# Optimization experiments

Hardware: AMD Instinct MI355X
Metric: run time of the kernel (lower is better)

Reference implementation:

```python
import jax, jax.numpy as jnp
import numpy as np

IMAGE_W = 1024
IMAGE_H = 1024
STRIDES = (8, 16, 32, 64, 128)
TOP_N = 1000
MIN_SCORE = 0.05
NMS_THR = 0.6
MAX_DET = 100
NEG = -1e9  # sentinel for suppressed scores


def _positions(stride):
    # Faithful to repo: shifts_x indexed by feature_h, shifts_y by feature_w,
    # grid built [hf, wf, 2] = [shift_x_i, shift_y_j], then permute(1,0,2).
    hf, wf = IMAGE_H // stride, IMAGE_W // stride
    sx = (jnp.arange(hf, dtype=jnp.float32) + 0.5) * stride
    sy = (jnp.arange(wf, dtype=jnp.float32) + 0.5) * stride
    pos = jnp.stack(jnp.meshgrid(sx, sy, indexing='ij'), axis=-1)  # [hf, wf, 2]
    return jnp.transpose(pos, (1, 0, 2)).reshape(-1, 2)  # [hf*wf, 2]


def _filter_level(cls_h, reg_h, ctr_h, pos):
    B, C = cls_h.shape[0], cls_h.shape[-1]
    cls_h = jax.nn.sigmoid(cls_h).reshape(B, -1, C)
    reg_h = jnp.exp(reg_h).reshape(B, -1, 4)
    ctr_h = jax.nn.sigmoid(ctr_h).reshape(B, -1)
    scores = jnp.max(cls_h, axis=-1)
    classes = jnp.argmax(cls_h, axis=-1).astype(jnp.int32)
    scores = jnp.sqrt(scores * ctr_h)
    N = scores.shape[1]
    if N >= TOP_N:
        scores, idx = jax.lax.top_k(scores, TOP_N)  # sorted descending, like torch.topk
        classes = jnp.take_along_axis(classes, idx, axis=1)
        reg_h = jnp.take_along_axis(reg_h, idx[..., None], axis=1)
        posb = pos[idx]  # [B, TOP_N, 2]
    else:
        posb = jnp.broadcast_to(pos[None], (B, N, 2))
    return scores, classes, reg_h, posb


def _snap(reg, pos):
    # reg: [B, N, 4] (l,t,r,b), pos: [B, N, 2]
    b = jnp.concatenate([pos - reg[:, :, 0:2], pos + reg[:, :, 2:4]], axis=-1)
    b = b.astype(jnp.int32)  # torch .int() truncation
    b = jnp.stack([
        jnp.maximum(b[..., 0], 0),
        jnp.maximum(b[..., 1], 0),
        jnp.minimum(b[..., 2], IMAGE_W - 1),
        jnp.minimum(b[..., 3], IMAGE_H - 1),
    ], axis=-1)
    return b.astype(jnp.float32)


def _nms_image(scores, classes, boxes):
    # scores [N], classes [N] int32, boxes [N,4] float (already snapped to int grid)
    s = jnp.where(scores > MIN_SCORE, scores, NEG)
    x1, y1, x2, y2 = boxes[:, 0], boxes[:, 1], boxes[:, 2], boxes[:, 3]
    areas = (x2 - x1) * (y2 - y1)
    out_s = -jnp.ones((MAX_DET,), jnp.float32)
    out_c = -jnp.ones((MAX_DET,), jnp.float32)
    out_b = -jnp.ones((MAX_DET, 4), jnp.float32)

    def body(i, st):
        s, os_, oc, ob = st
        idx = jnp.argmax(s)            # highest remaining score -> sorted keep order
        ok = s[idx] > MIN_SCORE        # any un-suppressed valid candidate left?
        bb = boxes[idx]
        iw = jnp.clip(jnp.minimum(x2, bb[2]) - jnp.maximum(x1, bb[0]), 0.0)
        ih = jnp.clip(jnp.minimum(y2, bb[3]) - jnp.maximum(y1, bb[1]), 0.0)
        inter = iw * ih
        iou = inter / (areas + areas[idx] - inter + 1e-12)
        s = jnp.where((iou > NMS_THR) & ok, NEG, s)
        s = s.at[idx].set(NEG)
        os_ = os_.at[i].set(jnp.where(ok, scores[idx], -1.0))
        oc = oc.at[i].set(jnp.where(ok, classes[idx].astype(jnp.float32), -1.0))
        ob = ob.at[i].set(jnp.where(ok, bb, -jnp.ones((4,), jnp.float32)))
        return (s, os_, oc, ob)

    _, os_, oc, ob = jax.lax.fori_loop(0, MAX_DET, body, (s, out_s, out_c, out_b))
    return os_, oc, ob


def _decode(cls_heads, reg_heads, ctr_heads):
    sc_l, cl_l, rg_l, ps_l = [], [], [], []
    for c, r, t, st in zip(cls_heads, reg_heads, ctr_heads, STRIDES):
        sc, cl, rg, ps = _filter_level(c, r, t, _positions(st))
        sc_l.append(sc); cl_l.append(cl); rg_l.append(rg); ps_l.append(ps)
    scores = jnp.concatenate(sc_l, axis=1)
    classes = jnp.concatenate(cl_l, axis=1)
    regs = jnp.concatenate(rg_l, axis=1)
    poss = jnp.concatenate(ps_l, axis=1)
    boxes = _snap(regs, poss)
    return jax.vmap(_nms_image)(scores, classes, boxes)


def setup_inputs() -> dict:
    key = jax.random.key(0)
    ks = jax.random.split(key, 15)
    B, C = 8, 80
    sizes = [IMAGE_H // s for s in STRIDES]
    inp = {}
    for i, hw in enumerate(sizes):
        inp[f'cls{i}'] = jax.random.normal(ks[i], (B, hw, hw, C), dtype=jnp.float32)
        # +3 so exp(reg) gives realistic ~20px extents
        inp[f'reg{i}'] = jax.random.normal(ks[5 + i], (B, hw, hw, 4), dtype=jnp.float32) + 3.0
        inp[f'ctr{i}'] = jax.random.normal(ks[10 + i], (B, hw, hw, 1), dtype=jnp.float32)
    return inp


def reference(cls0, cls1, cls2, cls3, cls4,
              reg0, reg1, reg2, reg3, reg4,
              ctr0, ctr1, ctr2, ctr3, ctr4):
    cls_heads = [cls0, cls1, cls2, cls3, cls4]
    reg_heads = [reg0, reg1, reg2, reg3, reg4]
    ctr_heads = [ctr0, ctr1, ctr2, ctr3, ctr4]
    batch_scores, batch_classes, batch_boxes = _decode(cls_heads, reg_heads, ctr_heads)
    return batch_scores, batch_classes, batch_boxes
```

## Files before the change

kernel.cpp:

```cpp
#include <hip/hip_runtime.h>

#define NPOS 21824
#define MINS 0.05f
#define BT   1024
#define NW   (BT/64)

struct Ptrs { const float* cls[5]; const float* reg[5]; const float* ctr[5]; };

__device__ __forceinline__ float sigf(float x){ return 1.0f/(1.0f+expf(-x)); }

__device__ __forceinline__ unsigned long long mkkey(unsigned int b, int p){
    return ((unsigned long long)b << 16) | (unsigned)(65535 - p);
}

__global__ __launch_bounds__(256) void k_score(Ptrs P, float* scoreAll, int* clsAll,
                                               float4* boxAll)
{
    int img  = blockIdx.y;
    int blk  = blockIdx.x;
    int tid  = threadIdx.x;
    int posb = tid >> 2;
    int l    = tid & 3;
    int p    = blk*64 + posb;
    int lvl, base, lw, stride;
    if (blk < 256)      { lvl=0; base=0;     lw=7; stride=8;   }
    else if (blk < 320) { lvl=1; base=16384; lw=6; stride=16;  }
    else if (blk < 336) { lvl=2; base=20480; lw=5; stride=32;  }
    else if (blk < 340) { lvl=3; base=21504; lw=4; stride=64;  }
    else                { lvl=4; base=21760; lw=3; stride=128; }
    int pl = p - base;
    int h = pl >> lw, w = pl & ((1<<lw)-1);
    long long lidx = (long long)img*(1<<(2*lw)) + pl;

    const float4* c4 = (const float4*)(P.cls[lvl] + lidx*80);
    float mx = -3.4e38f; int mi = 0;
#pragma unroll
    for (int j = 0; j < 5; ++j) {
        int k = j*4 + l;
        float4 v = c4[k];
        int cb = k*4;
        if (v.x > mx){mx=v.x; mi=cb;}
        if (v.y > mx){mx=v.y; mi=cb+1;}
        if (v.z > mx){mx=v.z; mi=cb+2;}
        if (v.w > mx){mx=v.w; mi=cb+3;}
    }
#pragma unroll
    for (int d = 1; d < 4; d <<= 1) {
        float omx = __shfl_xor(mx, d);
        int   omi = __shfl_xor(mi, d);
        if (omx > mx || (omx == mx && omi < mi)) { mx = omx; mi = omi; }
    }
    if (l == 0) {
        float ct = P.ctr[lvl][lidx];
        float sc = sqrtf(sigf(mx)*sigf(ct));
        float4 rg = ((const float4*)P.reg[lvl])[lidx];
        float x = (w + 0.5f)*(float)stride;
        float y = (h + 0.5f)*(float)stride;
        int ix1 = (int)(x - expf(rg.x));
        int iy1 = (int)(y - expf(rg.y));
        int ix2 = (int)(x + expf(rg.z));
        int iy2 = (int)(y + expf(rg.w));
        ix1 = max(ix1,0); iy1 = max(iy1,0);
        ix2 = min(ix2,1023); iy2 = min(iy2,1023);
        int o = img*NPOS + p;
        scoreAll[o] = sc;
        clsAll[o]   = mi;
        boxAll[o]   = make_float4((float)ix1,(float)iy1,(float)ix2,(float)iy2);
    }
}

__device__ void radix24(const unsigned int* vals, int N, int K,
                        int* histA, int* histB, int* wsum,
                        unsigned int* shPref, int* shK, int tid)
{
    for (int i = tid; i < N; i += BT)
        atomicAdd(&histA[vals[i] >> 19], 1);
    __syncthreads();
    {
        int lo = tid*2;
        int ls = histA[lo] + histA[lo+1];
        int lane = tid & 63, wv = tid >> 6;
        int v = ls;
#pragma unroll
        for (int off = 1; off < 64; off <<= 1) {
            int o = __shfl_down(v, off);
            if (lane + off < 64) v += o;
        }
        if (lane == 0) wsum[wv] = v;
        __syncthreads();
        int add = 0;
        for (int q = wv + 1; q < NW; ++q) add += wsum[q];
        int mine = v + add;
        int above = mine - ls;
        if (above < K && mine >= K) {
            if (above + histA[lo+1] >= K) { *shPref = (unsigned)(lo+1) << 19; *shK = K - above; }
            else { *shPref = (unsigned)lo << 19; *shK = K - above - histA[lo+1]; }
        }
        __syncthreads();
    }
    unsigned int pref = *shPref;
    int K2 = *shK;
    for (int i = tid; i < N; i += BT) {
        unsigned int b = vals[i];
        if ((b >> 19) == (pref >> 19)) atomicAdd(&histB[(b >> 8) & 2047], 1);
    }
    __syncthreads();
    {
        int lo = tid*2;
        int ls = histB[lo] + histB[lo+1];
        int lane = tid & 63, wv = tid >> 6;
        int v = ls;
#pragma unroll
        for (int off = 1; off < 64; off <<= 1) {
            int o = __shfl_down(v, off);
            if (lane + off < 64) v += o;
        }
        if (lane == 0) wsum[wv] = v;
        __syncthreads();
        int add = 0;
        for (int q = wv + 1; q < NW; ++q) add += wsum[q];
        int mine = v + add;
        int above = mine - ls;
        if (above < K2 && mine >= K2) {
            if (above + histB[lo+1] >= K2) { *shPref = pref | ((unsigned)(lo+1) << 8); *shK = K2 - above; }
            else { *shPref = pref | ((unsigned)lo << 8); *shK = K2 - above - histB[lo+1]; }
        }
        __syncthreads();
    }
}

__global__ __launch_bounds__(BT) void k_nms(const float* scoreAll,
                                            const float4* boxAll, const int* clsAll,
                                            float* out)
{
    __shared__ int histA[2048], histB[2048], wsum[NW];
    __shared__ unsigned int shPref;
    __shared__ int shK, tick, eqn;
    __shared__ unsigned long long eqKey[1024];
    __shared__ unsigned long long sel[256];
    __shared__ unsigned long long sorted[256];
    __shared__ float4 sBox[256];
    __shared__ float  sCls[256];
    __shared__ __align__(16) unsigned long long sRow[256][4];
    __shared__ int accIdx[100];
    __shared__ float4 accBox[100];
    __shared__ int shNaM, shNa;
    __shared__ unsigned long long shLast;

    int img = blockIdx.x, tid = threadIdx.x;
    const unsigned int* gs = (const unsigned int*)scoreAll + (long long)img*NPOS;
    const float4* gBox = boxAll + (long long)img*NPOS;
    const int*    gCls = clsAll + (long long)img*NPOS;

    float* outS = out + img*100;
    float* outC = out + 800 + img*100;
    float* outB = out + 1600 + img*400;

    for (int i = tid; i < 2048; i += BT) { histA[i] = 0; histB[i] = 0; }
    if (tid == 0) { tick = 0; eqn = 0; }
    __syncthreads();

    radix24(gs, NPOS, 256, histA, histB, wsum, &shPref, &shK, tid);
    unsigned int kth = shPref >> 8;
    int need = shK;
    for (int i = tid; i < NPOS; i += BT) {
        unsigned int b = gs[i], hb = b >> 8;
        if (hb > kth)       { int t = atomicAdd(&tick, 1); sel[t] = mkkey(b, i); }
        else if (hb == kth) { int t = atomicAdd(&eqn, 1); if (t < 1024) eqKey[t] = mkkey(b, i); }
    }
    __syncthreads();
    int m = eqn, nG = tick;
    if (m <= 1024) {
        for (int q = tid; q < m; q += BT) {
            unsigned long long kq = eqKey[q];
            int r = 0;
            for (int j = 0; j < m; ++j) r += (eqKey[j] > kq);
            if (r < need) sel[nG + r] = kq;
        }
    } else if (tid == 0) {
        unsigned long long last = ~0ULL;
        for (int c = 0; c < need; ++c) {
            unsigned long long best = 0;
            for (int i = 0; i < NPOS; ++i) {
                unsigned int b = gs[i];
                if ((b >> 8) == kth) {
                    unsigned long long k2 = mkkey(b, i);
                    if (k2 < last && k2 > best) best = k2;
                }
            }
            sel[nG + c] = best; last = best;
        }
    }
    __syncthreads();

    if (tid < 256) {
        unsigned long long k = sel[tid];
        int r = 0;
        for (int j = 0; j < 256; ++j) r += (sel[j] > k);
        sorted[r] = k;
    }
    __syncthreads();
    if (tid < 256) {
        int p = 65535 - (int)(sorted[tid] & 0xFFFF);
        sBox[tid] = gBox[p];
        sCls[tid] = (float)gCls[p];
    }

    float myScore = 0.f;
    if (tid < 256) myScore = __uint_as_float((unsigned int)(sorted[tid] >> 16));
    int nValid = __syncthreads_count(myScore > MINS ? 1 : 0);

    {
        int row = tid & 255, qq = tid >> 8;
        float4 bi = sBox[row];
        float  ai = (bi.z-bi.x)*(bi.w-bi.y);
        unsigned long long mv = 0;
#pragma unroll 8
        for (int jj = 0; jj < 64; ++jj) {
            int j = qq*64 + jj;
            float4 bj = sBox[j];
            float aj = (bj.z-bj.x)*(bj.w-bj.y);
            float iw = fmaxf(fminf(bj.z,bi.z)-fmaxf(bj.x,bi.x),0.f);
            float ih = fmaxf(fminf(bj.w,bi.w)-fmaxf(bj.y,bi.y),0.f);
            float in_ = iw*ih;
            bool s = (j > row) && (in_/(aj+ai-in_+1e-12f) > 0.6f);
            mv |= ((unsigned long long)s) << jj;
        }
        sRow[row][qq] = mv;
    }
    __syncthreads();

    if (tid == 0) {
        int na = 0;
        unsigned long long r0=0, r1=0, r2=0, r3=0;
#define FCOS_WBLK(RW, IB)                                                  \
        {                                                                  \
            int hi = nValid < ((IB)+1)*64 ? nValid : ((IB)+1)*64;          \
            for (int i = (IB)*64; i < hi && na < 100; ++i) {               \
                if ((RW >> (i - (IB)*64)) & 1ull) continue;                \
                accIdx[na++] = i;                                          \
                const ulonglong2* rp = (const ulonglong2*)sRow[i];         \
                ulonglong2 ra = rp[0], rb = rp[1];                         \
                r0 |= ra.x; r1 |= ra.y; r2 |= rb.x; r3 |= rb.y;            \
            }                                                              \
        }
        FCOS_WBLK(r0,0) FCOS_WBLK(r1,1) FCOS_WBLK(r2,2) FCOS_WBLK(r3,3)
#undef FCOS_WBLK
        shNaM = na; shNa = na;
    }
    __syncthreads();

    int naM = shNaM;
    if (naM < 100 && nValid == 256) {
        if (tid < naM) accBox[tid] = sBox[accIdx[tid]];
        if (tid == 0) shLast = sorted[255];
        __syncthreads();
        while (true) {
            if (shNa >= 100) break;
            unsigned long long last = shLast;
            unsigned long long bk = 0;
            for (int i = tid; i < NPOS; i += BT) {
                unsigned long long k2 = mkkey(gs[i], i);
                if (k2 < last && k2 > bk) bk = k2;
            }
#pragma unroll
            for (int off = 32; off > 0; off >>= 1) {
                unsigned long long o = __shfl_down(bk, off);
                if (o > bk) bk = o;
            }
            int lane = tid & 63, wv = tid >> 6;
            if (lane == 0) eqKey[wv] = bk;
            __syncthreads();
            if (tid == 0) {
                unsigned long long best = 0;
                for (int q = 0; q < NW; ++q) if (eqKey[q] > best) best = eqKey[q];
                shLast = best;
            }
            __syncthreads();
            unsigned long long ck = shLast;
            if (ck == 0ULL) break;
            float sc = __uint_as_float((unsigned int)(ck >> 16));
            if (!(sc > MINS)) break;
            int p = 65535 - (int)(ck & 0xFFFF);
            float4 bb = gBox[p];
            float ba = (bb.z-bb.x)*(bb.w-bb.y);
            int na = shNa;
            bool mySup = false;
            if (tid < na) {
                float4 ab = accBox[tid];
                float aa = (ab.z-ab.x)*(ab.w-ab.y);
                float iw = fmaxf(fminf(bb.z,ab.z)-fmaxf(bb.x,ab.x),0.f);
                float ih = fmaxf(fminf(bb.w,ab.w)-fmaxf(bb.y,ab.y),0.f);
                float in_ = iw*ih;
                mySup = in_/(ba+aa-in_+1e-12f) > 0.6f;
            }
            int supCnt = __syncthreads_count(mySup);
            if (supCnt == 0) {
                if (tid == 0) {
                    int na2 = shNa;
                    outS[na2] = sc;
                    outC[na2] = (float)gCls[p];
                    outB[4*na2+0]=bb.x; outB[4*na2+1]=bb.y;
                    outB[4*na2+2]=bb.z; outB[4*na2+3]=bb.w;
                    accBox[na2] = bb;
                    shNa = na2 + 1;
                }
            }
            __syncthreads();
        }
    }
    __syncthreads();

    {
        int naM2 = shNaM, naT = shNa;
        if (tid < 100) {
            if (tid < naM2) {
                int r = accIdx[tid];
                unsigned long long k = sorted[r];
                float4 b = sBox[r];
                outS[tid] = __uint_as_float((unsigned int)(k >> 16));
                outC[tid] = sCls[r];
                outB[4*tid+0]=b.x; outB[4*tid+1]=b.y;
                outB[4*tid+2]=b.z; outB[4*tid+3]=b.w;
            } else if (tid >= naT) {
                outS[tid] = -1.f; outC[tid] = -1.f;
                outB[4*tid+0]=-1.f; outB[4*tid+1]=-1.f;
                outB[4*tid+2]=-1.f; outB[4*tid+3]=-1.f;
            }
        }
    }
}

extern "C" void kernel_launch(void* const* d_in, const int* in_sizes, int n_in,
                              void* d_out, int out_size, void* d_ws, size_t ws_size,
                              hipStream_t stream) {
    Ptrs P;
    bool interleaved = (in_sizes[1] == 8 * 128 * 128 * 4);
    for (int i = 0; i < 5; ++i) {
        if (interleaved) {
            P.cls[i] = (const float*)d_in[3*i];
            P.reg[i] = (const float*)d_in[3*i + 1];
            P.ctr[i] = (const float*)d_in[3*i + 2];
        } else {
            P.cls[i] = (const float*)d_in[i];
            P.reg[i] = (const float*)d_in[5 + i];
            P.ctr[i] = (const float*)d_in[10 + i];
        }
    }

    char* wbase = (char*)d_ws;
    size_t off = 0;
    auto alloc = [&](size_t bytes) -> void* {
        void* r = wbase + off;
        off += (bytes + 255) & ~(size_t)255;
        return r;
    };
    float*  scoreAll = (float*)alloc((size_t)8 * NPOS * 4);
    int*    clsAll   = (int*)alloc((size_t)8 * NPOS * 4);
    float4* boxAll   = (float4*)alloc((size_t)8 * NPOS * 16);

    dim3 gA(341, 8);
    k_score <<<gA, 256, 0, stream>>>(P, scoreAll, clsAll, boxAll);
    k_nms   <<<8, BT, 0, stream>>>(scoreAll, boxAll, clsAll, (float*)d_out);
}
```

Measured before the change: 159.7 us.

## Prefilter high-score candidates into a compact list and compute boxes lazily

The scoring kernel now appends keys for positions whose score exceeds a fixed 0.85 threshold to a per-image candidate list via a global atomic. The NMS kernel then runs its radix top-K selection over that short list instead of scanning all 21824 scores, and falls back to the full scan when the list holds fewer than 256 entries or overflows. Boxes are no longer precomputed and stored for every position; they are decoded from the regression input only for the selected candidates. This cuts global writes and the single-block scan cost, at the price of atomics in the score kernel, an extra memset, and a threshold tuned to the score distribution (the fallback keeps results correct).

Measured after the change: 241.2 us. 1.51x slower.

```diff
diff --git a/kernel.cpp b/kernel.cpp
--- a/kernel.cpp
+++ b/kernel.cpp
@@ -4,6 +4,8 @@
 #define MINS 0.05f
 #define BT   1024
 #define NW   (BT/64)
+#define TFAST 0.85f
+#define CAP  16384
 
 struct Ptrs { const float* cls[5]; const float* reg[5]; const float* ctr[5]; };
 
@@ -13,8 +15,30 @@
     return ((unsigned long long)b << 16) | (unsigned)(65535 - p);
 }
 
+__device__ __forceinline__ float4 computeBox(const Ptrs& P, int img, int p){
+    int base, lw, stride, lvl;
+    if (p < 16384)      { lvl=0; base=0;     lw=7; stride=8;   }
+    else if (p < 20480) { lvl=1; base=16384; lw=6; stride=16;  }
+    else if (p < 21504) { lvl=2; base=20480; lw=5; stride=32;  }
+    else if (p < 21760) { lvl=3; base=21504; lw=4; stride=64;  }
+    else                { lvl=4; base=21760; lw=3; stride=128; }
+    int pl = p - base;
+    int h = pl >> lw, w = pl & ((1<<lw)-1);
+    long long lidx = (long long)img*(1<<(2*lw)) + pl;
+    float4 rg = ((const float4*)P.reg[lvl])[lidx];
+    float x = (w + 0.5f)*(float)stride;
+    float y = (h + 0.5f)*(float)stride;
+    int ix1 = (int)(x - expf(rg.x));
+    int iy1 = (int)(y - expf(rg.y));
+    int ix2 = (int)(x + expf(rg.z));
+    int iy2 = (int)(y + expf(rg.w));
+    ix1 = max(ix1,0); iy1 = max(iy1,0);
+    ix2 = min(ix2,1023); iy2 = min(iy2,1023);
+    return make_float4((float)ix1,(float)iy1,(float)ix2,(float)iy2);
+}
+
 __global__ __launch_bounds__(256) void k_score(Ptrs P, float* scoreAll, int* clsAll,
-                                               float4* boxAll)
+                                               unsigned long long* list, int* listCnt)
 {
     int img  = blockIdx.y;
     int blk  = blockIdx.x;
@@ -22,14 +46,13 @@
     int posb = tid >> 2;
     int l    = tid & 3;
     int p    = blk*64 + posb;
-    int lvl, base, lw, stride;
-    if (blk < 256)      { lvl=0; base=0;     lw=7; stride=8;   }
-    else if (blk < 320) { lvl=1; base=16384; lw=6; stride=16;  }
-    else if (blk < 336) { lvl=2; base=20480; lw=5; stride=32;  }
-    else if (blk < 340) { lvl=3; base=21504; lw=4; stride=64;  }
-    else                { lvl=4; base=21760; lw=3; stride=128; }
+    int lvl, base, lw;
+    if (blk < 256)      { lvl=0; base=0;     lw=7; }
+    else if (blk < 320) { lvl=1; base=16384; lw=6; }
+    else if (blk < 336) { lvl=2; base=20480; lw=5; }
+    else if (blk < 340) { lvl=3; base=21504; lw=4; }
+    else                { lvl=4; base=21760; lw=3; }
     int pl = p - base;
-    int h = pl >> lw, w = pl & ((1<<lw)-1);
     long long lidx = (long long)img*(1<<(2*lw)) + pl;
 
     const float4* c4 = (const float4*)(P.cls[lvl] + lidx*80);
@@ -53,85 +76,47 @@
     if (l == 0) {
         float ct = P.ctr[lvl][lidx];
         float sc = sqrtf(sigf(mx)*sigf(ct));
-        float4 rg = ((const float4*)P.reg[lvl])[lidx];
-        float x = (w + 0.5f)*(float)stride;
-        float y = (h + 0.5f)*(float)stride;
-        int ix1 = (int)(x - expf(rg.x));
-        int iy1 = (int)(y - expf(rg.y));
-        int ix2 = (int)(x + expf(rg.z));
-        int iy2 = (int)(y + expf(rg.w));
-        ix1 = max(ix1,0); iy1 = max(iy1,0);
-        ix2 = min(ix2,1023); iy2 = min(iy2,1023);
         int o = img*NPOS + p;
         scoreAll[o] = sc;
         clsAll[o]   = mi;
-        boxAll[o]   = make_float4((float)ix1,(float)iy1,(float)ix2,(float)iy2);
-    }
-}
-
-__device__ void radix24(const unsigned int* vals, int N, int K,
-                        int* histA, int* histB, int* wsum,
-                        unsigned int* shPref, int* shK, int tid)
+        if (sc > TFAST) {
+            int t = atomicAdd(&listCnt[img], 1);
+            if (t < CAP) list[(long long)img*CAP + t] = mkkey(__float_as_uint(sc), p);
+        }
+    }
+}
+
+__device__ void suffix_pick(const int* hist, int* wsum, int K,
+                            unsigned int prefBase, int shift,
+                            unsigned int* shPref, int* shK, int tid)
 {
-    for (int i = tid; i < N; i += BT)
-        atomicAdd(&histA[vals[i] >> 19], 1);
-    __syncthreads();
-    {
-        int lo = tid*2;
-        int ls = histA[lo] + histA[lo+1];
-        int lane = tid & 63, wv = tid >> 6;
-        int v = ls;
+    int lo = tid*2;
+    int h0 = hist[lo], h1 = hist[lo+1];
+    int ls = h0 + h1;
+    int lane = tid & 63, wv = tid >> 6;
+    int v = ls;
 #pragma unroll
-        for (int off = 1; off < 64; off <<= 1) {
-            int o = __shfl_down(v, off);
-            if (lane + off < 64) v += o;
-        }
-        if (lane == 0) wsum[wv] = v;
-        __syncthreads();
-        int add = 0;
-        for (int q = wv + 1; q < NW; ++q) add += wsum[q];
-        int mine = v + add;
-        int above = mine - ls;
-        if (above < K && mine >= K) {
-            if (above + histA[lo+1] >= K) { *shPref = (unsigned)(lo+1) << 19; *shK = K - above; }
-            else { *shPref = (unsigned)lo << 19; *shK = K - above - histA[lo+1]; }
-        }
-        __syncthreads();
-    }
-    unsigned int pref = *shPref;
-    int K2 = *shK;
-    for (int i = tid; i < N; i += BT) {
-        unsigned int b = vals[i];
-        if ((b >> 19) == (pref >> 19)) atomicAdd(&histB[(b >> 8) & 2047], 1);
-    }
-    __syncthreads();
-    {
-        int lo = tid*2;
-        int ls = histB[lo] + histB[lo+1];
-        int lane = tid & 63, wv = tid >> 6;
-        int v = ls;
-#pragma unroll
-        for (int off = 1; off < 64; off <<= 1) {
-            int o = __shfl_down(v, off);
-            if (lane + off < 64) v += o;
-        }
-        if (lane == 0) wsum[wv] = v;
-        __syncthreads();
-        int add = 0;
-        for (int q = wv + 1; q < NW; ++q) add += wsum[q];
-        int mine = v + add;
-        int above = mine - ls;
-        if (above < K2 && mine >= K2) {
-            if (above + histB[lo+1] >= K2) { *shPref = pref | ((unsigned)(lo+1) << 8); *shK = K2 - above; }
-            else { *shPref = pref | ((unsigned)lo << 8); *shK = K2 - above - histB[lo+1]; }
-        }
-        __syncthreads();
-    }
-}
-
-__global__ __launch_bounds__(BT) void k_nms(const float* scoreAll,
-                                            const float4* boxAll, const int* clsAll,
-                                            float* out)
+    for (int off = 1; off < 64; off <<= 1) {
+        int o = __shfl_down(v, off);
+        if (lane + off < 64) v += o;
+    }
+    if (lane == 0) wsum[wv] = v;
+    __syncthreads();
+    int add = 0;
+    for (int q = wv + 1; q < NW; ++q) add += wsum[q];
+    int mine = v + add;
+    int above = mine - ls;
+    if (above < K && mine >= K) {
+        if (above + h1 >= K) { *shPref = prefBase | ((unsigned)(lo+1) << shift); *shK = K - above; }
+        else                 { *shPref = prefBase | ((unsigned)lo << shift); *shK = K - above - h1; }
+    }
+    __syncthreads();
+}
+
+__global__ __launch_bounds__(BT) void k_nms(Ptrs P, const float* scoreAll,
+                                            const int* clsAll,
+                                            const unsigned long long* list,
+                                            const int* listCnt, float* out)
 {
     __shared__ int histA[2048], histB[2048], wsum[NW];
     __shared__ unsigned int shPref;
@@ -149,24 +134,62 @@
 
     int img = blockIdx.x, tid = threadIdx.x;
     const unsigned int* gs = (const unsigned int*)scoreAll + (long long)img*NPOS;
-    const float4* gBox = boxAll + (long long)img*NPOS;
-    const int*    gCls = clsAll + (long long)img*NPOS;
+    const int* gCls = clsAll + (long long)img*NPOS;
+    const unsigned long long* gl = list + (long long)img*CAP;
 
     float* outS = out + img*100;
     float* outC = out + 800 + img*100;
     float* outB = out + 1600 + img*400;
 
+    int cnt = listCnt[img];
+    bool fastPath = (cnt >= 256 && cnt <= CAP);
+
     for (int i = tid; i < 2048; i += BT) { histA[i] = 0; histB[i] = 0; }
     if (tid == 0) { tick = 0; eqn = 0; }
     __syncthreads();
 
-    radix24(gs, NPOS, 256, histA, histB, wsum, &shPref, &shK, tid);
-    unsigned int kth = shPref >> 8;
-    int need = shK;
-    for (int i = tid; i < NPOS; i += BT) {
-        unsigned int b = gs[i], hb = b >> 8;
-        if (hb > kth)       { int t = atomicAdd(&tick, 1); sel[t] = mkkey(b, i); }
-        else if (hb == kth) { int t = atomicAdd(&eqn, 1); if (t < 1024) eqKey[t] = mkkey(b, i); }
+    unsigned int kth; int need;
+    if (fastPath) {
+        for (int i = tid; i < cnt; i += BT)
+            atomicAdd(&histA[(unsigned)(gl[i] >> 35)], 1);
+        __syncthreads();
+        suffix_pick(histA, wsum, 256, 0u, 19, &shPref, &shK, tid);
+        unsigned int pref = shPref; int K2 = shK;
+        for (int i = tid; i < cnt; i += BT) {
+            unsigned long long k = gl[i];
+            if ((unsigned)(k >> 35) == (pref >> 19))
+                atomicAdd(&histB[(unsigned)(k >> 24) & 2047], 1);
+        }
+        __syncthreads();
+        suffix_pick(histB, wsum, K2, pref, 8, &shPref, &shK, tid);
+        kth = shPref >> 8; need = shK;
+        for (int i = tid; i < cnt; i += BT) {
+            unsigned long long k = gl[i];
+            unsigned int hb = (unsigned)(k >> 24);
+            if (hb > kth)       { int t = atomicAdd(&tick, 1); sel[t] = k; }
+            else if (hb == kth) { int t = atomicAdd(&eqn, 1); if (t < 1024) eqKey[t] = k; }
+        }
+    } else {
+#pragma unroll 4
+        for (int i = tid; i < NPOS; i += BT)
+            atomicAdd(&histA[gs[i] >> 19], 1);
+        __syncthreads();
+        suffix_pick(histA, wsum, 256, 0u, 19, &shPref, &shK, tid);
+        unsigned int pref = shPref; int K2 = shK;
+#pragma unroll 4
+        for (int i = tid; i < NPOS; i += BT) {
+            unsigned int b = gs[i];
+            if ((b >> 19) == (pref >> 19)) atomicAdd(&histB[(b >> 8) & 2047], 1);
+        }
+        __syncthreads();
+        suffix_pick(histB, wsum, K2, pref, 8, &shPref, &shK, tid);
+        kth = shPref >> 8; need = shK;
+#pragma unroll 4
+        for (int i = tid; i < NPOS; i += BT) {
+            unsigned int b = gs[i], hb = b >> 8;
+            if (hb > kth)       { int t = atomicAdd(&tick, 1); sel[t] = mkkey(b, i); }
+            else if (hb == kth) { int t = atomicAdd(&eqn, 1); if (t < 1024) eqKey[t] = mkkey(b, i); }
+        }
     }
     __syncthreads();
     int m = eqn, nG = tick;
@@ -181,11 +204,18 @@
         unsigned long long last = ~0ULL;
         for (int c = 0; c < need; ++c) {
             unsigned long long best = 0;
-            for (int i = 0; i < NPOS; ++i) {
-                unsigned int b = gs[i];
-                if ((b >> 8) == kth) {
-                    unsigned long long k2 = mkkey(b, i);
-                    if (k2 < last && k2 > best) best = k2;
+            if (fastPath) {
+                for (int i = 0; i < cnt; ++i) {
+                    unsigned long long k2 = gl[i];
+                    if ((unsigned)(k2 >> 24) == kth && k2 < last && k2 > best) best = k2;
+                }
+            } else {
+                for (int i = 0; i < NPOS; ++i) {
+                    unsigned int b = gs[i];
+                    if ((b >> 8) == kth) {
+                        unsigned long long k2 = mkkey(b, i);
+                        if (k2 < last && k2 > best) best = k2;
+                    }
                 }
             }
             sel[nG + c] = best; last = best;
@@ -202,7 +232,7 @@
     __syncthreads();
     if (tid < 256) {
         int p = 65535 - (int)(sorted[tid] & 0xFFFF);
-        sBox[tid] = gBox[p];
+        sBox[tid] = computeBox(P, img, p);
         sCls[tid] = (float)gCls[p];
     }
 
@@ -282,7 +312,7 @@
             float sc = __uint_as_float((unsigned int)(ck >> 16));
             if (!(sc > MINS)) break;
             int p = 65535 - (int)(ck & 0xFFFF);
-            float4 bb = gBox[p];
+            float4 bb = computeBox(P, img, p);
             float ba = (bb.z-bb.x)*(bb.w-bb.y);
             int na = shNa;
             bool mySup = false;
@@ -355,11 +385,14 @@
         off += (bytes + 255) & ~(size_t)255;
         return r;
     };
-    float*  scoreAll = (float*)alloc((size_t)8 * NPOS * 4);
-    int*    clsAll   = (int*)alloc((size_t)8 * NPOS * 4);
-    float4* boxAll   = (float4*)alloc((size_t)8 * NPOS * 16);
+    float*              scoreAll = (float*)alloc((size_t)8 * NPOS * 4);
+    int*                clsAll   = (int*)alloc((size_t)8 * NPOS * 4);
+    unsigned long long* list     = (unsigned long long*)alloc((size_t)8 * CAP * 8);
+    int*                listCnt  = (int*)alloc((size_t)8 * 4);
+
+    hipMemsetAsync(listCnt, 0, 8 * sizeof(int), stream);
 
     dim3 gA(341, 8);
-    k_score <<<gA, 256, 0, stream>>>(P, scoreAll, clsAll, boxAll);
-    k_nms   <<<8, BT, 0, stream>>>(scoreAll, boxAll, clsAll, (float*)d_out);
-}
+    k_score <<<gA, 256, 0, stream>>>(P, scoreAll, clsAll, list, listCnt);
+    k_nms   <<<8, BT, 0, stream>>>(P, scoreAll, clsAll, list, listCnt, (float*)d_out);
+}
```
